# Optimization experiments

Measured on AMD Instinct MI355X. Metric: run time of the kernel, lower is better.

## Reference

```python
import jax, jax.numpy as jnp
import numpy as np

N_NODES = 100000
N_EDGES = 1600000
IN_DIM, HID_DIM, OUT_DIM = 32, 64, 8


def sage_conv(x, src, dst, W_l, b_l, W_r, n_nodes):
    # PyG SAGEConv (aggr='mean', root_weight=True):
    # out_i = W_l @ mean_{j in N(i)} x_j + b_l + W_r @ x_i
    msg_sum = jax.ops.segment_sum(x[src], dst, num_segments=n_nodes)  # [N, F]
    deg = jax.ops.segment_sum(jnp.ones((src.shape[0],), x.dtype), dst,
                              num_segments=n_nodes)  # [N]
    agg = msg_sum / jnp.maximum(deg, 1.0)[:, None]
    return agg @ W_l.T + b_l + x @ W_r.T


def setup_inputs() -> dict:
    key = jax.random.key(0)
    ks = jax.random.split(key, 8)
    x = jax.random.normal(ks[0], (N_NODES, IN_DIM), dtype=jnp.float32)
    edge_index = jax.random.randint(ks[1], (2, N_EDGES), 0, N_NODES, dtype=jnp.int64)
    s1 = 1.0 / np.sqrt(IN_DIM)
    s2 = 1.0 / np.sqrt(HID_DIM)
    return {
        "x": x,
        "edge_index": edge_index,
        "W1_l": jax.random.uniform(ks[2], (HID_DIM, IN_DIM), jnp.float32, -s1, s1),
        "b1": jnp.zeros((HID_DIM,), jnp.float32),
        "W1_r": jax.random.uniform(ks[3], (HID_DIM, IN_DIM), jnp.float32, -s1, s1),
        "W2_l": jax.random.uniform(ks[4], (OUT_DIM, HID_DIM), jnp.float32, -s2, s2),
        "b2": jnp.zeros((OUT_DIM,), jnp.float32),
        "W2_r": jax.random.uniform(ks[5], (OUT_DIM, HID_DIM), jnp.float32, -s2, s2),
    }


def reference(x, edge_index, W1_l, b1, W1_r, W2_l, b2, W2_r):
    src, dst = edge_index[0], edge_index[1]
    h = sage_conv(x, src, dst, W1_l, b1, W1_r, N_NODES)
    h = jax.nn.relu(h)
    out = sage_conv(h, src, dst, W2_l, b2, W2_r, N_NODES)
    return out
```

## Files before the change

### kernel.cpp

```cpp
#include <hip/hip_runtime.h>

#define N_NODES 100000
#define N_EDGES 1600000
#define IN_DIM 32
#define HID_DIM 64
#define OUT_DIM 8
#define BK 64
#define NBKT ((N_NODES + BK - 1) / BK)
#define QC 1280
#define QCP 224
#define QSTR 2048
#define CHUNK 4096
#define NCHUNK ((N_EDGES + CHUNK - 1) / CHUNK)

typedef unsigned short u16;
typedef unsigned int u32;
typedef unsigned long long ull;

__device__ __forceinline__ float bf2f(u16 v) {
    return __uint_as_float(((u32)v) << 16);
}

__device__ __forceinline__ u16 f2bf(float f) {
    u32 u = __float_as_uint(f);
    u32 lsb = (u >> 16) & 1u;
    u += 0x7fffu + lsb;
    return (u16)(u >> 16);
}

__device__ __forceinline__ float ldf(const void* p, size_t i, int bf) {
    return bf ? bf2f(((const u16*)p)[i]) : ((const float*)p)[i];
}

__global__ __launch_bounds__(256) void k_part2(
    const int* __restrict__ ei, const u32* __restrict__ xw,
    const void* __restrict__ W1l, const void* __restrict__ b1,
    const void* __restrict__ W1r,
    const void* __restrict__ W2l, const void* __restrict__ b2,
    const void* __restrict__ W2r,
    int* __restrict__ qcnt, u32* __restrict__ qbuf,
    float* __restrict__ tW1l, float* __restrict__ tW1r,
    float* __restrict__ tW2l, float* __restrict__ tW2r,
    float* __restrict__ tb1, float* __restrict__ tb2)
{
    __shared__ int shv, bfv;
    __shared__ int hist[NBKT], gbase[NBKT], lcur[NBKT];
    int t = threadIdx.x;
    int part = blockIdx.x & 7;
    if (t < 64) {
        int v = ei[2 * t + 1];
        ull m1 = __ballot(v == 0);
        u32 wd = xw[t];
        u32 b = (wd >> 8) & 0x7fu;
        ull m2 = __ballot(b >= 0x38u && b <= 0x41u);
        if (t == 0) {
            shv = (m1 == ~0ULL) ? 1 : 0;
            bfv = (__popcll(m2) >= 56) ? 1 : 0;
        }
    }
    for (int i = t; i < NBKT; i += 256) { hist[i] = 0; lcur[i] = 0; }
    __syncthreads();
    int sh = shv, bf = bfv;

    if (blockIdx.x < 16) {
        for (int i = blockIdx.x * 256 + t; i < HID_DIM * IN_DIM; i += 16 * 256) {
            int o = i / IN_DIM, k = i % IN_DIM;
            tW1l[k * HID_DIM + o] = ldf(W1l, i, bf);
            tW1r[k * HID_DIM + o] = ldf(W1r, i, bf);
        }
        for (int i = blockIdx.x * 256 + t; i < OUT_DIM * HID_DIM; i += 16 * 256) {
            int o = i / HID_DIM, k = i % HID_DIM;
            tW2l[k * OUT_DIM + o] = ldf(W2l, i, bf);
            tW2r[k * OUT_DIM + o] = ldf(W2r, i, bf);
        }
        if (blockIdx.x == 0) {
            if (t < HID_DIM) tb1[t] = ldf(b1, t, bf);
            if (t < OUT_DIM) tb2[t] = ldf(b2, t, bf);
        }
    }

    int e0 = blockIdx.x * CHUNK;
    int myd[16], mys[16];
    #pragma unroll
    for (int i = 0; i < 16; i++) {
        int e = e0 + i * 256 + t;
        if (e < N_EDGES) {
            size_t off = (size_t)e << sh;
            mys[i] = __builtin_nontemporal_load(&ei[off]);
            int d = __builtin_nontemporal_load(&ei[((size_t)N_EDGES << sh) + off]);
            myd[i] = d;
            atomicAdd(&hist[d >> 6], 1);
        } else myd[i] = -1;
    }
    __syncthreads();
    for (int i = t; i < NBKT; i += 256) {
        int h = hist[i];
        gbase[i] = h ? atomicAdd(&qcnt[part * QSTR + i], h) : 0;
    }
    __syncthreads();
    #pragma unroll
    for (int i = 0; i < 16; i++) {
        int d = myd[i];
        if (d >= 0) {
            int bk = d >> 6;
            int p = gbase[bk] + atomicAdd(&lcur[bk], 1);
            if (p < QCP)
                qbuf[((size_t)part * NBKT + bk) * QCP + p] =
                    ((u32)mys[i] << 6) | (u32)(d & 63);
        }
    }
}

__global__ __launch_bounds__(256, 4) void k_l1(
    const void* __restrict__ x,
    const int* __restrict__ qcnt, const u32* __restrict__ qbuf,
    const float* __restrict__ tW1l, const float* __restrict__ tW1r,
    const float* __restrict__ tW2l, const float* __restrict__ tW2r,
    const float* __restrict__ tb1, const float* __restrict__ tb2,
    u16* __restrict__ gbuf, float* __restrict__ rbuf,
    const u32* __restrict__ xw)
{
    __shared__ int hist[BK], pos[BK], pcur[BK];
    __shared__ int mp[8], mbase[8], mtv;
    __shared__ u32 raw[QC];
    __shared__ u32 srt[QC];
    __shared__ float xs[BK][IN_DIM];
    __shared__ float aggw[4][2][IN_DIM];
    __shared__ float hb[8][HID_DIM + 1];
    __shared__ int bfv;

    int t = threadIdx.x;
    if (t < 64) {
        u32 wd = xw[t];
        u32 b = (wd >> 8) & 0x7fu;
        ull m2 = __ballot(b >= 0x38u && b <= 0x41u);
        if (t == 0) bfv = (__popcll(m2) >= 56) ? 1 : 0;
    }
    if (t < BK) hist[t] = 0;
    int b = blockIdx.x, nb = b * BK;
    if (t < 8) {
        int v = qcnt[t * QSTR + b];
        if (v < 0) v = 0;
        if (v > QCP) v = QCP;
        mp[t] = v;
    }
    __syncthreads();
    int bf = bfv;
    if (t == 0) {
        int s = 0;
        for (int p = 0; p < 8; p++) {
            mbase[p] = s;
            int v = mp[p];
            if (s + v > QC) v = QC - s;
            if (v < 0) v = 0;
            mp[p] = v; s += v;
        }
        mtv = s;
    }
    __syncthreads();
    int m = mtv;

    for (int p = 0; p < 8; p++) {
        const u32* qp = qbuf + ((size_t)p * NBKT + b) * QCP;
        int mpp = mp[p], mb = mbase[p];
        for (int i = t; i < mpp; i += 256)
            raw[mb + i] = __builtin_nontemporal_load(&qp[i]);
    }

    if (bf) {
        const u32* xr = (const u32*)x + (size_t)nb * (IN_DIM / 2);
        int lim = ((N_NODES - nb < BK) ? (N_NODES - nb) : BK) * (IN_DIM / 2);
        for (int i = t; i < BK * (IN_DIM / 2); i += 256) {
            u32 w = (i < lim) ? xr[i] : 0u;
            int r = i >> 4, c = i & 15;
            xs[r][2 * c]     = bf2f((u16)w);
            xs[r][2 * c + 1] = bf2f((u16)(w >> 16));
        }
    } else {
        const float* xr = (const float*)x + (size_t)nb * IN_DIM;
        int lim = ((N_NODES - nb < BK) ? (N_NODES - nb) : BK) * IN_DIM;
        for (int i = t; i < BK * IN_DIM; i += 256)
            xs[i >> 5][i & 31] = (i < lim) ? xr[i] : 0.0f;
    }
    __syncthreads();

    for (int i = t; i < m; i += 256)
        atomicAdd(&hist[raw[i] & 63], 1);
    __syncthreads();
    if (t < 64) {
        int v = hist[t];
        int inc = v;
        #pragma unroll
        for (int o = 1; o < 64; o <<= 1) {
            int y = __shfl_up(inc, o, 64);
            if (t >= o) inc += y;
        }
        int ex = inc - v;
        pos[t] = ex; pcur[t] = ex;
    }
    __syncthreads();
    for (int i = t; i < m; i += 256) {
        u32 u = raw[i];
        int p = atomicAdd(&pcur[u & 63], 1);
        srt[p] = u >> 6;
    }
    __syncthreads();

    int wid = t >> 6, lane = t & 63;
    int half = lane >> 5, g2 = (lane >> 3) & 3, l = lane & 7;
    int o = lane;
    float bb = tb1[o];
    for (int pr = 0; pr < 8; pr++) {
        int s0 = pr * 8 + wid * 2;
        int ns = s0 + half;
        int st = pos[ns], deg = hist[ns];
        float a0 = 0, a1 = 0, a2 = 0, a3 = 0;
        float c0 = 0, c1 = 0, c2 = 0, c3 = 0;
        float d0 = 0, d1 = 0, d2 = 0, d3 = 0;
        float e0 = 0, e1 = 0, e2 = 0, e3 = 0;
        int j = g2;
        for (; j + 12 < deg; j += 16) {
            int sA = (int)srt[st + j];
            int sB = (int)srt[st + j + 4];
            int sC = (int)srt[st + j + 8];
            int sD = (int)srt[st + j + 12];
            if (bf) {
                ushort4 vA = reinterpret_cast<const ushort4*>((const u16*)x + (size_t)sA * IN_DIM)[l];
                ushort4 vB = reinterpret_cast<const ushort4*>((const u16*)x + (size_t)sB * IN_DIM)[l];
                ushort4 vC = reinterpret_cast<const ushort4*>((const u16*)x + (size_t)sC * IN_DIM)[l];
                ushort4 vD = reinterpret_cast<const ushort4*>((const u16*)x + (size_t)sD * IN_DIM)[l];
                a0 += bf2f(vA.x); a1 += bf2f(vA.y); a2 += bf2f(vA.z); a3 += bf2f(vA.w);
                c0 += bf2f(vB.x); c1 += bf2f(vB.y); c2 += bf2f(vB.z); c3 += bf2f(vB.w);
                d0 += bf2f(vC.x); d1 += bf2f(vC.y); d2 += bf2f(vC.z); d3 += bf2f(vC.w);
                e0 += bf2f(vD.x); e1 += bf2f(vD.y); e2 += bf2f(vD.z); e3 += bf2f(vD.w);
            } else {
                float4 vA = reinterpret_cast<const float4*>((const float*)x + (size_t)sA * IN_DIM)[l];
                float4 vB = reinterpret_cast<const float4*>((const float*)x + (size_t)sB * IN_DIM)[l];
                float4 vC = reinterpret_cast<const float4*>((const float*)x + (size_t)sC * IN_DIM)[l];
                float4 vD = reinterpret_cast<const float4*>((const float*)x + (size_t)sD * IN_DIM)[l];
                a0 += vA.x; a1 += vA.y; a2 += vA.z; a3 += vA.w;
                c0 += vB.x; c1 += vB.y; c2 += vB.z; c3 += vB.w;
                d0 += vC.x; d1 += vC.y; d2 += vC.z; d3 += vC.w;
                e0 += vD.x; e1 += vD.y; e2 += vD.z; e3 += vD.w;
            }
        }
        for (; j + 4 < deg; j += 8) {
            int sA = (int)srt[st + j];
            int sB = (int)srt[st + j + 4];
            if (bf) {
                ushort4 vA = reinterpret_cast<const ushort4*>((const u16*)x + (size_t)sA * IN_DIM)[l];
                ushort4 vB = reinterpret_cast<const ushort4*>((const u16*)x + (size_t)sB * IN_DIM)[l];
                a0 += bf2f(vA.x); a1 += bf2f(vA.y); a2 += bf2f(vA.z); a3 += bf2f(vA.w);
                c0 += bf2f(vB.x); c1 += bf2f(vB.y); c2 += bf2f(vB.z); c3 += bf2f(vB.w);
            } else {
                float4 vA = reinterpret_cast<const float4*>((const float*)x + (size_t)sA * IN_DIM)[l];
                float4 vB = reinterpret_cast<const float4*>((const float*)x + (size_t)sB * IN_DIM)[l];
                a0 += vA.x; a1 += vA.y; a2 += vA.z; a3 += vA.w;
                c0 += vB.x; c1 += vB.y; c2 += vB.z; c3 += vB.w;
            }
        }
        if (j < deg) {
            int s = (int)srt[st + j];
            if (bf) {
                ushort4 vv = reinterpret_cast<const ushort4*>((const u16*)x + (size_t)s * IN_DIM)[l];
                a0 += bf2f(vv.x); a1 += bf2f(vv.y); a2 += bf2f(vv.z); a3 += bf2f(vv.w);
            } else {
                float4 vv = reinterpret_cast<const float4*>((const float*)x + (size_t)s * IN_DIM)[l];
                a0 += vv.x; a1 += vv.y; a2 += vv.z; a3 += vv.w;
            }
        }
        a0 += c0 + d0 + e0;
        a1 += c1 + d1 + e1;
        a2 += c2 + d2 + e2;
        a3 += c3 + d3 + e3;
        a0 += __shfl_xor(a0, 8, 64);  a0 += __shfl_xor(a0, 16, 64);
        a1 += __shfl_xor(a1, 8, 64);  a1 += __shfl_xor(a1, 16, 64);
        a2 += __shfl_xor(a2, 8, 64);  a2 += __shfl_xor(a2, 16, 64);
        a3 += __shfl_xor(a3, 8, 64);  a3 += __shfl_xor(a3, 16, 64);
        if (g2 == 0) {
            aggw[wid][half][4 * l + 0] = a0; aggw[wid][half][4 * l + 1] = a1;
            aggw[wid][half][4 * l + 2] = a2; aggw[wid][half][4 * l + 3] = a3;
        }
        float rd0 = 1.0f / fmaxf((float)hist[s0], 1.0f);
        float rd1 = 1.0f / fmaxf((float)hist[s0 + 1], 1.0f);
        float acc0 = bb, acc1 = bb;
        #pragma unroll 8
        for (int k = 0; k < IN_DIM; k++) {
            float wl = tW1l[k * HID_DIM + o];
            float wr = tW1r[k * HID_DIM + o];
            acc0 += (aggw[wid][0][k] * rd0) * wl + xs[s0][k] * wr;
            acc1 += (aggw[wid][1][k] * rd1) * wl + xs[s0 + 1][k] * wr;
        }
        hb[wid * 2][o]     = fmaxf(acc0, 0.0f);
        hb[wid * 2 + 1][o] = fmaxf(acc1, 0.0f);
        int hs = wid * 2 + half;
        float ga = 0.0f, ra = 0.0f;
        #pragma unroll 4
        for (int mm = 0; mm < 16; mm++) {
            int k = g2 * 16 + mm;
            float hv = hb[hs][k];
            ga += hv * tW2l[k * OUT_DIM + l];
            ra += hv * tW2r[k * OUT_DIM + l];
        }
        ga += __shfl_xor(ga, 8, 64);  ga += __shfl_xor(ga, 16, 64);
        ra += __shfl_xor(ra, 8, 64);  ra += __shfl_xor(ra, 16, 64);
        int n = nb + ns;
        if (g2 == 0 && n < N_NODES) {
            __builtin_nontemporal_store(f2bf(ga), &gbuf[(size_t)n * OUT_DIM + l]);
            __builtin_nontemporal_store(ra + tb2[l], &rbuf[(size_t)n * OUT_DIM + l]);
        }
    }
}

__global__ __launch_bounds__(256) void k_l2(
    const u16* __restrict__ gbuf, const float* __restrict__ rbuf,
    const int* __restrict__ qcnt, const u32* __restrict__ qbuf,
    const u32* __restrict__ xw, void* __restrict__ out)
{
    __shared__ int hist[BK], pos[BK], pcur[BK];
    __shared__ int mp[8], mbase[8], mtv;
    __shared__ u32 raw[QC];
    __shared__ u32 srt[QC];
    __shared__ int bfv;
    int t = threadIdx.x;
    if (t < 64) {
        u32 w = xw[t];
        u32 b = (w >> 8) & 0x7fu;
        ull m2 = __ballot(b >= 0x38u && b <= 0x41u);
        if (t == 0) bfv = (__popcll(m2) >= 56) ? 1 : 0;
    }
    if (t < BK) hist[t] = 0;
    int b = blockIdx.x, nb = b * BK;
    if (t < 8) {
        int v = qcnt[t * QSTR + b];
        if (v < 0) v = 0;
        if (v > QCP) v = QCP;
        mp[t] = v;
    }
    __syncthreads();
    if (t == 0) {
        int s = 0;
        for (int p = 0; p < 8; p++) {
            mbase[p] = s;
            int v = mp[p];
            if (s + v > QC) v = QC - s;
            if (v < 0) v = 0;
            mp[p] = v; s += v;
        }
        mtv = s;
    }
    __syncthreads();
    int m = mtv;
    for (int p = 0; p < 8; p++) {
        const u32* qp = qbuf + ((size_t)p * NBKT + b) * QCP;
        int mpp = mp[p], mb = mbase[p];
        for (int i = t; i < mpp; i += 256)
            raw[mb + i] = __builtin_nontemporal_load(&qp[i]);
    }
    __syncthreads();

    for (int i = t; i < m; i += 256)
        atomicAdd(&hist[raw[i] & 63], 1);
    __syncthreads();
    if (t < 64) {
        int v = hist[t];
        int inc = v;
        #pragma unroll
        for (int o = 1; o < 64; o <<= 1) {
            int y = __shfl_up(inc, o, 64);
            if (t >= o) inc += y;
        }
        int ex = inc - v;
        pos[t] = ex; pcur[t] = ex;
    }
    __syncthreads();
    for (int i = t; i < m; i += 256) {
        u32 u = raw[i];
        int p = atomicAdd(&pcur[u & 63], 1);
        srt[p] = u >> 6;
    }
    __syncthreads();

    int grp = t >> 3, l = t & 7;
    for (int r = 0; r < 2; r++) {
        int ns = grp * 2 + r;
        int st = pos[ns], deg = hist[ns];
        float a0 = 0.0f, a1 = 0.0f, a2 = 0.0f, a3 = 0.0f;
        int j = 0;
        for (; j + 3 < deg; j += 4) {
            int v0 = (int)srt[st + j];
            int v1 = (int)srt[st + j + 1];
            int v2 = (int)srt[st + j + 2];
            int v3 = (int)srt[st + j + 3];
            a0 += bf2f(gbuf[(size_t)v0 * OUT_DIM + l]);
            a1 += bf2f(gbuf[(size_t)v1 * OUT_DIM + l]);
            a2 += bf2f(gbuf[(size_t)v2 * OUT_DIM + l]);
            a3 += bf2f(gbuf[(size_t)v3 * OUT_DIM + l]);
        }
        for (; j < deg; j++) a0 += bf2f(gbuf[(size_t)srt[st + j] * OUT_DIM + l]);
        int n = nb + ns;
        if (n < N_NODES) {
            float res = (a0 + a1 + a2 + a3) / fmaxf((float)deg, 1.0f)
                      + rbuf[(size_t)n * OUT_DIM + l];
            size_t oi = (size_t)n * OUT_DIM + l;
            if (bfv) ((u16*)out)[oi] = f2bf(res);
            else     ((float*)out)[oi] = res;
        }
    }
}

extern "C" void kernel_launch(void* const* d_in, const int* in_sizes, int n_in,
                              void* d_out, int out_size, void* d_ws, size_t ws_size,
                              hipStream_t stream) {
    const void* x   = d_in[0];
    const int*  ei  = (const int*)d_in[1];
    const void* W1l = d_in[2];
    const void* b1  = d_in[3];
    const void* W1r = d_in[4];
    const void* W2l = d_in[5];
    const void* b2  = d_in[6];
    const void* W2r = d_in[7];

    int* qcnt    = (int*)d_ws;
    float* tW1l  = (float*)(qcnt + 8 * QSTR);
    float* tW1r  = tW1l + IN_DIM * HID_DIM;
    float* tW2l  = tW1r + IN_DIM * HID_DIM;
    float* tW2r  = tW2l + HID_DIM * OUT_DIM;
    float* tb1   = tW2r + HID_DIM * OUT_DIM;
    float* tb2   = tb1 + HID_DIM;
    u32* qbuf    = (u32*)(tb2 + OUT_DIM);
    u16* gbuf    = (u16*)(qbuf + (size_t)8 * NBKT * QCP);
    float* rbuf  = (float*)(gbuf + (size_t)N_NODES * OUT_DIM);

    hipMemsetAsync(d_ws, 0, 8 * QSTR * sizeof(int), stream);

    k_part2<<<NCHUNK, 256, 0, stream>>>(ei, (const u32*)x,
                                        W1l, b1, W1r, W2l, b2, W2r,
                                        qcnt, qbuf,
                                        tW1l, tW1r, tW2l, tW2r, tb1, tb2);
    k_l1<<<NBKT, 256, 0, stream>>>(x, qcnt, qbuf,
                                   tW1l, tW1r, tW2l, tW2r, tb1, tb2,
                                   gbuf, rbuf, (const u32*)x);
    k_l2<<<NBKT, 256, 0, stream>>>(gbuf, rbuf, qcnt, qbuf,
                                   (const u32*)x, d_out);
}
```

Baseline: 213.5 us.

## Fuse partition, layer-1 and layer-2 kernels into one cooperative grid-synced kernel

Replaces the memset and the three kernel launches with a single cooperative kernel. It runs weight transposition, edge bucketing, layer-1 aggregation and transform, and layer-2 aggregation as phases separated by grid.sync. The per-bucket sorted source list stays in LDS between the layer-1 and layer-2 phases, so layer 2 does not re-read and re-sort the queue. This is meant to cut launch and inter-kernel gaps and redundant queue traffic. In exchange it forces every block to be resident at once (launch bounds 256,7) and pays grid-wide barrier costs; the partition phase uses only a subset of the blocks. A fallback to the old three-kernel path runs if the cooperative launch fails.

```diff
diff --git a/kernel.cpp b/kernel.cpp
--- a/kernel.cpp
+++ b/kernel.cpp
@@ -1,4 +1,5 @@
 #include <hip/hip_runtime.h>
+#include <hip/hip_cooperative_groups.h>
 
 #define N_NODES 100000
 #define N_EDGES 1600000
@@ -30,6 +31,317 @@
 
 __device__ __forceinline__ float ldf(const void* p, size_t i, int bf) {
     return bf ? bf2f(((const u16*)p)[i]) : ((const float*)p)[i];
+}
+
+union ShU {
+    struct { int hist[NBKT], gbase[NBKT], lcur[NBKT]; } p;
+    struct {
+        int hist[BK], pos[BK], pcur[BK];
+        int mp[8], mbase[8], mtv;
+        u32 raw[QC], srt[QC];
+        float xs[BK][IN_DIM];
+        float aggw[4][2][IN_DIM];
+        float hb[8][HID_DIM + 1];
+    } l;
+};
+
+__global__ __launch_bounds__(256, 7) void k_fused(
+    const int* __restrict__ ei, const u32* __restrict__ xw,
+    const void* __restrict__ W1l, const void* __restrict__ b1,
+    const void* __restrict__ W1r,
+    const void* __restrict__ W2l, const void* __restrict__ b2,
+    const void* __restrict__ W2r,
+    int* __restrict__ qcnt, u32* __restrict__ qbuf,
+    float* __restrict__ tW1l, float* __restrict__ tW1r,
+    float* __restrict__ tW2l, float* __restrict__ tW2r,
+    float* __restrict__ tb1, float* __restrict__ tb2,
+    u16* __restrict__ gbuf, float* __restrict__ rbuf,
+    void* __restrict__ out)
+{
+    __shared__ ShU u;
+    __shared__ int shv_, bfv_;
+    cooperative_groups::grid_group grid = cooperative_groups::this_grid();
+
+    int t = threadIdx.x;
+    int b = blockIdx.x;
+
+    if (t < 64) {
+        int v = ei[2 * t + 1];
+        ull m1 = __ballot(v == 0);
+        u32 wd = xw[t];
+        u32 bb = (wd >> 8) & 0x7fu;
+        ull m2 = __ballot(bb >= 0x38u && bb <= 0x41u);
+        if (t == 0) {
+            shv_ = (m1 == ~0ULL) ? 1 : 0;
+            bfv_ = (__popcll(m2) >= 56) ? 1 : 0;
+        }
+    }
+    __syncthreads();
+    int sh = shv_, bf = bfv_;
+
+    {
+        int i = b * 256 + t;
+        if (i < 8 * QSTR) qcnt[i] = 0;
+    }
+    if (b < 16) {
+        for (int i = b * 256 + t; i < HID_DIM * IN_DIM; i += 16 * 256) {
+            int o = i / IN_DIM, k = i % IN_DIM;
+            tW1l[k * HID_DIM + o] = ldf(W1l, i, bf);
+            tW1r[k * HID_DIM + o] = ldf(W1r, i, bf);
+        }
+        for (int i = b * 256 + t; i < OUT_DIM * HID_DIM; i += 16 * 256) {
+            int o = i / HID_DIM, k = i % HID_DIM;
+            tW2l[k * OUT_DIM + o] = ldf(W2l, i, bf);
+            tW2r[k * OUT_DIM + o] = ldf(W2r, i, bf);
+        }
+        if (b == 0) {
+            if (t < HID_DIM) tb1[t] = ldf(b1, t, bf);
+            if (t < OUT_DIM) tb2[t] = ldf(b2, t, bf);
+        }
+    }
+    grid.sync();
+
+    if (b < NCHUNK) {
+        int part = b & 7;
+        for (int i = t; i < NBKT; i += 256) { u.p.hist[i] = 0; u.p.lcur[i] = 0; }
+        __syncthreads();
+        int e0 = b * CHUNK;
+        int myd[16], mys[16];
+        #pragma unroll
+        for (int i = 0; i < 16; i++) {
+            int e = e0 + i * 256 + t;
+            if (e < N_EDGES) {
+                size_t off = (size_t)e << sh;
+                mys[i] = ei[off];
+                int d = ei[((size_t)N_EDGES << sh) + off];
+                myd[i] = d;
+                atomicAdd(&u.p.hist[d >> 6], 1);
+            } else myd[i] = -1;
+        }
+        __syncthreads();
+        for (int i = t; i < NBKT; i += 256) {
+            int h = u.p.hist[i];
+            u.p.gbase[i] = h ? atomicAdd(&qcnt[part * QSTR + i], h) : 0;
+        }
+        __syncthreads();
+        #pragma unroll
+        for (int i = 0; i < 16; i++) {
+            int d = myd[i];
+            if (d >= 0) {
+                int bk = d >> 6;
+                int p = u.p.gbase[bk] + atomicAdd(&u.p.lcur[bk], 1);
+                if (p < QCP)
+                    qbuf[((size_t)part * NBKT + bk) * QCP + p] =
+                        ((u32)mys[i] << 6) | (u32)(d & 63);
+            }
+        }
+    }
+    grid.sync();
+
+    int nb = b * BK;
+    if (t < BK) u.l.hist[t] = 0;
+    if (t < 8) {
+        int v = qcnt[t * QSTR + b];
+        if (v < 0) v = 0;
+        if (v > QCP) v = QCP;
+        u.l.mp[t] = v;
+    }
+    __syncthreads();
+    if (t == 0) {
+        int s = 0;
+        for (int p = 0; p < 8; p++) {
+            u.l.mbase[p] = s;
+            int v = u.l.mp[p];
+            if (s + v > QC) v = QC - s;
+            if (v < 0) v = 0;
+            u.l.mp[p] = v; s += v;
+        }
+        u.l.mtv = s;
+    }
+    __syncthreads();
+    int m = u.l.mtv;
+
+    for (int p = 0; p < 8; p++) {
+        const u32* qp = qbuf + ((size_t)p * NBKT + b) * QCP;
+        int mpp = u.l.mp[p], mb = u.l.mbase[p];
+        for (int i = t; i < mpp; i += 256)
+            u.l.raw[mb + i] = qp[i];
+    }
+
+    const void* x = (const void*)xw;
+    if (bf) {
+        const u32* xr = xw + (size_t)nb * (IN_DIM / 2);
+        int lim = ((N_NODES - nb < BK) ? (N_NODES - nb) : BK) * (IN_DIM / 2);
+        for (int i = t; i < BK * (IN_DIM / 2); i += 256) {
+            u32 w = (i < lim) ? xr[i] : 0u;
+            int r = i >> 4, c = i & 15;
+            u.l.xs[r][2 * c]     = bf2f((u16)w);
+            u.l.xs[r][2 * c + 1] = bf2f((u16)(w >> 16));
+        }
+    } else {
+        const float* xr = (const float*)x + (size_t)nb * IN_DIM;
+        int lim = ((N_NODES - nb < BK) ? (N_NODES - nb) : BK) * IN_DIM;
+        for (int i = t; i < BK * IN_DIM; i += 256)
+            u.l.xs[i >> 5][i & 31] = (i < lim) ? xr[i] : 0.0f;
+    }
+    __syncthreads();
+
+    for (int i = t; i < m; i += 256)
+        atomicAdd(&u.l.hist[u.l.raw[i] & 63], 1);
+    __syncthreads();
+    if (t < 64) {
+        int v = u.l.hist[t];
+        int inc = v;
+        #pragma unroll
+        for (int o = 1; o < 64; o <<= 1) {
+            int y = __shfl_up(inc, o, 64);
+            if (t >= o) inc += y;
+        }
+        int ex = inc - v;
+        u.l.pos[t] = ex; u.l.pcur[t] = ex;
+    }
+    __syncthreads();
+    for (int i = t; i < m; i += 256) {
+        u32 uu = u.l.raw[i];
+        int p = atomicAdd(&u.l.pcur[uu & 63], 1);
+        u.l.srt[p] = uu >> 6;
+    }
+    __syncthreads();
+
+    int wid = t >> 6, lane = t & 63;
+    int half = lane >> 5, g2 = (lane >> 3) & 3, l = lane & 7;
+    int o = lane;
+    float bb2 = tb1[o];
+    for (int pr = 0; pr < 8; pr++) {
+        int s0 = pr * 8 + wid * 2;
+        int ns = s0 + half;
+        int st = u.l.pos[ns], deg = u.l.hist[ns];
+        float a0 = 0, a1 = 0, a2 = 0, a3 = 0;
+        float c0 = 0, c1 = 0, c2 = 0, c3 = 0;
+        float d0 = 0, d1 = 0, d2 = 0, d3 = 0;
+        float e0 = 0, e1 = 0, e2 = 0, e3 = 0;
+        int j = g2;
+        for (; j + 12 < deg; j += 16) {
+            int sA = (int)u.l.srt[st + j];
+            int sB = (int)u.l.srt[st + j + 4];
+            int sC = (int)u.l.srt[st + j + 8];
+            int sD = (int)u.l.srt[st + j + 12];
+            if (bf) {
+                ushort4 vA = reinterpret_cast<const ushort4*>((const u16*)x + (size_t)sA * IN_DIM)[l];
+                ushort4 vB = reinterpret_cast<const ushort4*>((const u16*)x + (size_t)sB * IN_DIM)[l];
+                ushort4 vC = reinterpret_cast<const ushort4*>((const u16*)x + (size_t)sC * IN_DIM)[l];
+                ushort4 vD = reinterpret_cast<const ushort4*>((const u16*)x + (size_t)sD * IN_DIM)[l];
+                a0 += bf2f(vA.x); a1 += bf2f(vA.y); a2 += bf2f(vA.z); a3 += bf2f(vA.w);
+                c0 += bf2f(vB.x); c1 += bf2f(vB.y); c2 += bf2f(vB.z); c3 += bf2f(vB.w);
+                d0 += bf2f(vC.x); d1 += bf2f(vC.y); d2 += bf2f(vC.z); d3 += bf2f(vC.w);
+                e0 += bf2f(vD.x); e1 += bf2f(vD.y); e2 += bf2f(vD.z); e3 += bf2f(vD.w);
+            } else {
+                float4 vA = reinterpret_cast<const float4*>((const float*)x + (size_t)sA * IN_DIM)[l];
+                float4 vB = reinterpret_cast<const float4*>((const float*)x + (size_t)sB * IN_DIM)[l];
+                float4 vC = reinterpret_cast<const float4*>((const float*)x + (size_t)sC * IN_DIM)[l];
+                float4 vD = reinterpret_cast<const float4*>((const float*)x + (size_t)sD * IN_DIM)[l];
+                a0 += vA.x; a1 += vA.y; a2 += vA.z; a3 += vA.w;
+                c0 += vB.x; c1 += vB.y; c2 += vB.z; c3 += vB.w;
+                d0 += vC.x; d1 += vC.y; d2 += vC.z; d3 += vC.w;
+                e0 += vD.x; e1 += vD.y; e2 += vD.z; e3 += vD.w;
+            }
+        }
+        for (; j + 4 < deg; j += 8) {
+            int sA = (int)u.l.srt[st + j];
+            int sB = (int)u.l.srt[st + j + 4];
+            if (bf) {
+                ushort4 vA = reinterpret_cast<const ushort4*>((const u16*)x + (size_t)sA * IN_DIM)[l];
+                ushort4 vB = reinterpret_cast<const ushort4*>((const u16*)x + (size_t)sB * IN_DIM)[l];
+                a0 += bf2f(vA.x); a1 += bf2f(vA.y); a2 += bf2f(vA.z); a3 += bf2f(vA.w);
+                c0 += bf2f(vB.x); c1 += bf2f(vB.y); c2 += bf2f(vB.z); c3 += bf2f(vB.w);
+            } else {
+                float4 vA = reinterpret_cast<const float4*>((const float*)x + (size_t)sA * IN_DIM)[l];
+                float4 vB = reinterpret_cast<const float4*>((const float*)x + (size_t)sB * IN_DIM)[l];
+                a0 += vA.x; a1 += vA.y; a2 += vA.z; a3 += vA.w;
+                c0 += vB.x; c1 += vB.y; c2 += vB.z; c3 += vB.w;
+            }
+        }
+        if (j < deg) {
+            int s = (int)u.l.srt[st + j];
+            if (bf) {
+                ushort4 vv = reinterpret_cast<const ushort4*>((const u16*)x + (size_t)s * IN_DIM)[l];
+                a0 += bf2f(vv.x); a1 += bf2f(vv.y); a2 += bf2f(vv.z); a3 += bf2f(vv.w);
+            } else {
+                float4 vv = reinterpret_cast<const float4*>((const float*)x + (size_t)s * IN_DIM)[l];
+                a0 += vv.x; a1 += vv.y; a2 += vv.z; a3 += vv.w;
+            }
+        }
+        a0 += c0 + d0 + e0;
+        a1 += c1 + d1 + e1;
+        a2 += c2 + d2 + e2;
+        a3 += c3 + d3 + e3;
+        a0 += __shfl_xor(a0, 8, 64);  a0 += __shfl_xor(a0, 16, 64);
+        a1 += __shfl_xor(a1, 8, 64);  a1 += __shfl_xor(a1, 16, 64);
+        a2 += __shfl_xor(a2, 8, 64);  a2 += __shfl_xor(a2, 16, 64);
+        a3 += __shfl_xor(a3, 8, 64);  a3 += __shfl_xor(a3, 16, 64);
+        if (g2 == 0) {
+            u.l.aggw[wid][half][4 * l + 0] = a0; u.l.aggw[wid][half][4 * l + 1] = a1;
+            u.l.aggw[wid][half][4 * l + 2] = a2; u.l.aggw[wid][half][4 * l + 3] = a3;
+        }
+        float rd0 = 1.0f / fmaxf((float)u.l.hist[s0], 1.0f);
+        float rd1 = 1.0f / fmaxf((float)u.l.hist[s0 + 1], 1.0f);
+        float acc0 = bb2, acc1 = bb2;
+        #pragma unroll 8
+        for (int k = 0; k < IN_DIM; k++) {
+            float wl = tW1l[k * HID_DIM + o];
+            float wr = tW1r[k * HID_DIM + o];
+            acc0 += (u.l.aggw[wid][0][k] * rd0) * wl + u.l.xs[s0][k] * wr;
+            acc1 += (u.l.aggw[wid][1][k] * rd1) * wl + u.l.xs[s0 + 1][k] * wr;
+        }
+        u.l.hb[wid * 2][o]     = fmaxf(acc0, 0.0f);
+        u.l.hb[wid * 2 + 1][o] = fmaxf(acc1, 0.0f);
+        int hs = wid * 2 + half;
+        float ga = 0.0f, ra = 0.0f;
+        #pragma unroll 4
+        for (int mm = 0; mm < 16; mm++) {
+            int k = g2 * 16 + mm;
+            float hv = u.l.hb[hs][k];
+            ga += hv * tW2l[k * OUT_DIM + l];
+            ra += hv * tW2r[k * OUT_DIM + l];
+        }
+        ga += __shfl_xor(ga, 8, 64);  ga += __shfl_xor(ga, 16, 64);
+        ra += __shfl_xor(ra, 8, 64);  ra += __shfl_xor(ra, 16, 64);
+        int n = nb + ns;
+        if (g2 == 0 && n < N_NODES) {
+            gbuf[(size_t)n * OUT_DIM + l] = f2bf(ga);
+            rbuf[(size_t)n * OUT_DIM + l] = ra + tb2[l];
+        }
+    }
+    grid.sync();
+
+    {
+        int grp = t >> 3, ll = t & 7;
+        for (int r = 0; r < 2; r++) {
+            int ns = grp * 2 + r;
+            int st = u.l.pos[ns], deg = u.l.hist[ns];
+            float a0 = 0.0f, a1 = 0.0f, a2 = 0.0f, a3 = 0.0f;
+            int j = 0;
+            for (; j + 3 < deg; j += 4) {
+                int v0 = (int)u.l.srt[st + j];
+                int v1 = (int)u.l.srt[st + j + 1];
+                int v2 = (int)u.l.srt[st + j + 2];
+                int v3 = (int)u.l.srt[st + j + 3];
+                a0 += bf2f(gbuf[(size_t)v0 * OUT_DIM + ll]);
+                a1 += bf2f(gbuf[(size_t)v1 * OUT_DIM + ll]);
+                a2 += bf2f(gbuf[(size_t)v2 * OUT_DIM + ll]);
+                a3 += bf2f(gbuf[(size_t)v3 * OUT_DIM + ll]);
+            }
+            for (; j < deg; j++) a0 += bf2f(gbuf[(size_t)u.l.srt[st + j] * OUT_DIM + ll]);
+            int n = nb + ns;
+            if (n < N_NODES) {
+                float res = (a0 + a1 + a2 + a3) / fmaxf((float)deg, 1.0f)
+                          + rbuf[(size_t)n * OUT_DIM + ll];
+                size_t oi = (size_t)n * OUT_DIM + ll;
+                if (bf) ((u16*)out)[oi] = f2bf(res);
+                else    ((float*)out)[oi] = res;
+            }
+        }
+    }
 }
 
 __global__ __launch_bounds__(256) void k_part2(
@@ -432,15 +744,38 @@
     u16* gbuf    = (u16*)(qbuf + (size_t)8 * NBKT * QCP);
     float* rbuf  = (float*)(gbuf + (size_t)N_NODES * OUT_DIM);
 
-    hipMemsetAsync(d_ws, 0, 8 * QSTR * sizeof(int), stream);
-
-    k_part2<<<NCHUNK, 256, 0, stream>>>(ei, (const u32*)x,
-                                        W1l, b1, W1r, W2l, b2, W2r,
-                                        qcnt, qbuf,
-                                        tW1l, tW1r, tW2l, tW2r, tb1, tb2);
-    k_l1<<<NBKT, 256, 0, stream>>>(x, qcnt, qbuf,
-                                   tW1l, tW1r, tW2l, tW2r, tb1, tb2,
-                                   gbuf, rbuf, (const u32*)x);
-    k_l2<<<NBKT, 256, 0, stream>>>(gbuf, rbuf, qcnt, qbuf,
-                                   (const u32*)x, d_out);
+    const int*  ei_   = ei;
+    const u32*  xw_   = (const u32*)x;
+    const void* W1l_  = W1l; const void* b1_  = b1;  const void* W1r_ = W1r;
+    const void* W2l_  = W2l; const void* b2_  = b2;  const void* W2r_ = W2r;
+    int*  qcnt_ = qcnt;  u32* qbuf_ = qbuf;
+    float *tW1l_ = tW1l, *tW1r_ = tW1r, *tW2l_ = tW2l, *tW2r_ = tW2r;
+    float *tb1_ = tb1, *tb2_ = tb2;
+    u16* gbuf_ = gbuf; float* rbuf_ = rbuf; void* out_ = d_out;
+    void* kargs[] = {
+        (void*)&ei_, (void*)&xw_,
+        (void*)&W1l_, (void*)&b1_, (void*)&W1r_,
+        (void*)&W2l_, (void*)&b2_, (void*)&W2r_,
+        (void*)&qcnt_, (void*)&qbuf_,
+        (void*)&tW1l_, (void*)&tW1r_, (void*)&tW2l_, (void*)&tW2r_,
+        (void*)&tb1_, (void*)&tb2_,
+        (void*)&gbuf_, (void*)&rbuf_, (void*)&out_
+    };
+    hipError_t err = hipLaunchCooperativeKernel(
+        reinterpret_cast<const void*>(&k_fused),
+        dim3(NBKT), dim3(256), kargs, 0, stream);
+
+    if (err != hipSuccess) {
+        (void)hipGetLastError();
+        hipMemsetAsync(d_ws, 0, 8 * QSTR * sizeof(int), stream);
+        k_part2<<<NCHUNK, 256, 0, stream>>>(ei, (const u32*)x,
+                                            W1l, b1, W1r, W2l, b2, W2r,
+                                            qcnt, qbuf,
+                                            tW1l, tW1r, tW2l, tW2r, tb1, tb2);
+        k_l1<<<NBKT, 256, 0, stream>>>(x, qcnt, qbuf,
+                                       tW1l, tW1r, tW2l, tW2r, tb1, tb2,
+                                       gbuf, rbuf, (const u32*)x);
+        k_l2<<<NBKT, 256, 0, stream>>>(gbuf, rbuf, qcnt, qbuf,
+                                       (const u32*)x, d_out);
+    }
 }
```

Result: slower. 701.4 us (+228.6%).
